# Kernel tuning notes

Hardware: AMD Instinct MI355X
Metric: run time of the kernel (lower is better)

Reference implementation:

```python
import jax, jax.numpy as jnp
import numpy as np

N = 65536      # num ref nodes
M = 65536      # num query nodes
E = 1572864    # num edges (avg degree 24)
K0 = 27        # num kernels (3x3x3 neighborhood)
D1 = 64        # input channels
D2 = 64        # output channels


def setup_inputs() -> dict:
    key = jax.random.key(0)
    k1, k2, k3, k4, k5, k6 = jax.random.split(key, 6)
    # kernel init mirrors initialize_kernel_weight (uniform in [-bound, bound])
    fan_in = D1 * K0
    gain = float(np.sqrt(2.0 / (1.0 + 5.0)))  # leaky_relu gain with slope sqrt(5)
    std = gain / np.sqrt(fan_in)
    bound = float(np.sqrt(3.0) * std)
    kernel = jax.random.uniform(k1, (K0, D1, D2), minval=-bound, maxval=bound, dtype=jnp.float32)
    ref_feat = jax.random.normal(k2, (N, D1), dtype=jnp.float32)
    e_kernel = jax.random.randint(k3, (E,), 0, K0)
    e_ref = jax.random.randint(k4, (E,), 0, N)
    e_query = jax.random.randint(k5, (E,), 0, M)
    e_weight = jax.random.uniform(k6, (E,), dtype=jnp.float32)
    return {
        "kernel": kernel,
        "ref_feat": ref_feat,
        "e_kernel": e_kernel,
        "e_ref": e_ref,
        "e_query": e_query,
        "num_queries": M,
        "e_weight": e_weight,
    }


def reference(kernel, ref_feat, e_kernel, e_ref, e_query, num_queries, e_weight):
    # Math of MessagePassing.forward:
    #   query_feat[m] = sum_{edges e: e_query[e]==m} w_e * (ref_feat[e_ref[e]] @ kernel[e_kernel[e]])
    # Efficient form: precompute each node's transform under every kernel
    # (N*K0*D1*D2 dense GEMM), then gather per edge and scatter-reduce.
    transformed = jnp.einsum('nd,kdo->nko', ref_feat, kernel)   # [N, K0, D2]
    msgs = transformed[e_ref, e_kernel] * e_weight[:, None]      # [E, D2]
    query_feat = jax.ops.segment_sum(msgs, e_query, num_segments=num_queries)  # [M, D2]
    return query_feat
```

## Files before the change

kernel.cpp:

```cpp
#include <hip/hip_runtime.h>

#define DIN 64
#define DOUT 64
#define MAXK 32

typedef __bf16 bf16x8 __attribute__((ext_vector_type(8)));
typedef float  f32x4  __attribute__((ext_vector_type(4)));

static __device__ inline unsigned short f2b(float x) {
    return __builtin_bit_cast(unsigned short, (__bf16)x);
}
static __device__ inline float b2f(unsigned short u) {
    return __uint_as_float(((unsigned int)u) << 16);
}


__global__ void conv_w_kernel(const float* __restrict__ W,
                              unsigned short* __restrict__ Wt, int total) {
    int i = blockIdx.x * blockDim.x + threadIdx.x;
    if (i < total) {
        int j    = i & 7;
        int lane = (i >> 3) & 63;
        int h    = (i >> 9) & 1;
        int t    = (i >> 10) & 3;
        int k    = i >> 12;
        int col  = lane & 15;
        int quad = lane >> 4;
        int d1 = h * 32 + quad * 8 + j;
        int d2 = t * 16 + col;
        Wt[i] = f2b(W[(k * 64 + d1) * 64 + d2]);
    }
}


__global__ __launch_bounds__(256) void phaseA_kernel(
    const float* __restrict__ ref,
    const unsigned short* __restrict__ Wt,
    unsigned short* __restrict__ T,
    int K0, int Nn)
{
    const int lane = threadIdx.x & 63;
    const int wid  = threadIdx.x >> 6;
    const int col  = lane & 15;
    const int quad = lane >> 4;
    const int n0   = blockIdx.x * 64 + wid * 16;
    const int row  = n0 + col;

    __shared__ __align__(16) char ldsbuf[4][16 * 144];
    char* buf = ldsbuf[wid];

    const float* rp = ref + (size_t)row * 64;
    f32x4 r0 = *reinterpret_cast<const f32x4*>(rp + quad * 8);
    f32x4 r1 = *reinterpret_cast<const f32x4*>(rp + quad * 8 + 4);
    f32x4 r2 = *reinterpret_cast<const f32x4*>(rp + 32 + quad * 8);
    f32x4 r3 = *reinterpret_cast<const f32x4*>(rp + 32 + quad * 8 + 4);
    bf16x8 b0, b1;
    #pragma unroll
    for (int i = 0; i < 4; ++i) {
        b0[i]     = (__bf16)r0[i];
        b0[4 + i] = (__bf16)r1[i];
        b1[i]     = (__bf16)r2[i];
        b1[4 + i] = (__bf16)r3[i];
    }

    const int rrow = lane >> 2;
    const int rq   = lane & 3;

    for (int k = 0; k < K0; ++k) {
        const unsigned short* Wk = Wt + (size_t)k * 4096;
        #pragma unroll
        for (int t = 0; t < 4; ++t) {
            const unsigned short* ap = Wk + (size_t)t * 1024 + lane * 8;
            bf16x8 a0 = *reinterpret_cast<const bf16x8*>(ap);
            bf16x8 a1 = *reinterpret_cast<const bf16x8*>(ap + 512);
            f32x4 c = {0.f, 0.f, 0.f, 0.f};
            c = __builtin_amdgcn_mfma_f32_16x16x32_bf16(a0, b0, c, 0, 0, 0);
            c = __builtin_amdgcn_mfma_f32_16x16x32_bf16(a1, b1, c, 0, 0, 0);
            unsigned int lo = (unsigned int)f2b(c[0]) | ((unsigned int)f2b(c[1]) << 16);
            unsigned int hi = (unsigned int)f2b(c[2]) | ((unsigned int)f2b(c[3]) << 16);
            *reinterpret_cast<uint2*>(buf + col * 144 + t * 32 + quad * 8) =
                make_uint2(lo, hi);
        }
        uint4 v0 = *reinterpret_cast<const uint4*>(buf + rrow * 144 + rq * 32);
        uint4 v1 = *reinterpret_cast<const uint4*>(buf + rrow * 144 + rq * 32 + 16);
        size_t gbase = ((size_t)k * Nn + n0 + rrow) * 64 + rq * 16;
        *reinterpret_cast<uint4*>(T + gbase)     = v0;
        *reinterpret_cast<uint4*>(T + gbase + 8) = v1;
    }
}


__global__ void p1_hist_kernel(const int* __restrict__ eq, int E,
                               int* __restrict__ qcount) {
    __shared__ int l[256];
    l[threadIdx.x] = 0;
    __syncthreads();
    int stride = gridDim.x * blockDim.x;
    for (int i = blockIdx.x * blockDim.x + threadIdx.x; i < E; i += stride)
        atomicAdd(&l[((unsigned)eq[i]) >> 8], 1);
    __syncthreads();
    int v = l[threadIdx.x];
    if (v) atomicAdd(&qcount[threadIdx.x], v);
}

__global__ void p1_scan_kernel(const int* __restrict__ qcount,
                               int* __restrict__ gbase, int* __restrict__ gcursor,
                               int* __restrict__ qstart, int NB, int M, int E) {
    __shared__ int sh[256];
    int t = threadIdx.x;
    int v = (t < NB) ? qcount[t] : 0;
    sh[t] = v;
    __syncthreads();
    #pragma unroll
    for (int o = 1; o < 256; o <<= 1) {
        int x = (t >= o) ? sh[t - o] : 0;
        __syncthreads();
        sh[t] += x;
        __syncthreads();
    }
    int ex = sh[t] - v;
    if (t < NB) { gbase[t] = ex; gcursor[t] = ex; }
    if (t == 0) qstart[M] = E;
}

__global__ __launch_bounds__(256) void p1_scatter_kernel(
    const int* __restrict__ eq, const int* __restrict__ er,
    const int* __restrict__ ek, const float* __restrict__ ew,
    int E, int* __restrict__ gcursor, uint2* __restrict__ tmp)
{
    __shared__ int bin[256];
    __shared__ int base[256];
    const int t = threadIdx.x;
    bin[t] = 0;
    __syncthreads();
    const int i0 = blockIdx.x * 4096;
    unsigned key[16];
    unsigned rank[16];
    uint2 pay[16];
    #pragma unroll
    for (int u = 0; u < 16; ++u) {
        int i = i0 + u * 256 + t;
        if (i < E) {
            int q = eq[i];
            unsigned b = ((unsigned)q) >> 8;
            key[u] = b;
            rank[u] = atomicAdd(&bin[b], 1);
            pay[u] = make_uint2((unsigned)er[i] | ((unsigned)ek[i] << 16) |
                                ((unsigned)(q & 255) << 21),
                                __float_as_uint(ew[i]));
        } else {
            key[u] = 0xFFFFFFFFu;
        }
    }
    __syncthreads();
    int c = bin[t];
    if (c) base[t] = atomicAdd(&gcursor[t], c);
    __syncthreads();
    #pragma unroll
    for (int u = 0; u < 16; ++u) {
        if (key[u] != 0xFFFFFFFFu)
            tmp[(size_t)base[key[u]] + rank[u]] = pay[u];
    }
}

__global__ __launch_bounds__(256) void p2_kernel(
    const uint2* __restrict__ tmp, const int* __restrict__ gbase,
    const int* __restrict__ qcount, uint2* __restrict__ rec,
    int* __restrict__ qstart)
{
    __shared__ int fine[256];
    __shared__ int foff[256];
    const int b = blockIdx.x;
    const int t = threadIdx.x;
    const int s = gbase[b];
    const int L = qcount[b];
    fine[t] = 0;
    __syncthreads();
    for (int i = t; i < L; i += 256)
        atomicAdd(&fine[(tmp[s + i].x >> 21) & 255], 1);
    __syncthreads();
    int v = fine[t];
    __syncthreads();
    #pragma unroll
    for (int o = 1; o < 256; o <<= 1) {
        int x = (t >= o) ? fine[t - o] : 0;
        __syncthreads();
        fine[t] += x;
        __syncthreads();
    }
    foff[t] = fine[t] - v;
    qstart[b * 256 + t] = s + foff[t];
    __syncthreads();
    fine[t] = 0;
    __syncthreads();
    for (int i = t; i < L; i += 256) {
        uint2 p = tmp[s + i];
        unsigned fb = (p.x >> 21) & 255;
        int r = atomicAdd(&fine[fb], 1);
        rec[(size_t)s + foff[fb] + r] = p;
    }
}


__global__ __launch_bounds__(256) void phaseB_kernel(
    const unsigned short* __restrict__ T,
    const uint2* __restrict__ rec,
    const int* __restrict__ qstart,
    float* __restrict__ out, int Nn)
{
    const int lane = threadIdx.x & 63;
    const int wid  = threadIdx.x >> 6;
    const int q    = blockIdx.x * 4 + wid;

    int beg = qstart[q];
    int end = qstart[q + 1];
    float acc = 0.f;

    int j = beg;
    for (; j + 3 < end; j += 4) {
        uint2 v0 = rec[j];
        uint2 v1 = rec[j + 1];
        uint2 v2 = rec[j + 2];
        uint2 v3 = rec[j + 3];
        unsigned m0 = __builtin_amdgcn_readfirstlane(v0.x);
        unsigned m1 = __builtin_amdgcn_readfirstlane(v1.x);
        unsigned m2 = __builtin_amdgcn_readfirstlane(v2.x);
        unsigned m3 = __builtin_amdgcn_readfirstlane(v3.x);
        float w0 = __uint_as_float(__builtin_amdgcn_readfirstlane(v0.y));
        float w1 = __uint_as_float(__builtin_amdgcn_readfirstlane(v1.y));
        float w2 = __uint_as_float(__builtin_amdgcn_readfirstlane(v2.y));
        float w3 = __uint_as_float(__builtin_amdgcn_readfirstlane(v3.y));
        unsigned short t0 = T[((size_t)((m0 >> 16) & 31) * Nn + (m0 & 0xFFFFu)) * 64 + lane];
        unsigned short t1 = T[((size_t)((m1 >> 16) & 31) * Nn + (m1 & 0xFFFFu)) * 64 + lane];
        unsigned short t2 = T[((size_t)((m2 >> 16) & 31) * Nn + (m2 & 0xFFFFu)) * 64 + lane];
        unsigned short t3 = T[((size_t)((m3 >> 16) & 31) * Nn + (m3 & 0xFFFFu)) * 64 + lane];
        acc = fmaf(w0, b2f(t0), acc);
        acc = fmaf(w1, b2f(t1), acc);
        acc = fmaf(w2, b2f(t2), acc);
        acc = fmaf(w3, b2f(t3), acc);
    }
    for (; j < end; ++j) {
        uint2 v0 = rec[j];
        unsigned m0 = __builtin_amdgcn_readfirstlane(v0.x);
        float w0 = __uint_as_float(__builtin_amdgcn_readfirstlane(v0.y));
        acc = fmaf(w0, b2f(T[((size_t)((m0 >> 16) & 31) * Nn + (m0 & 0xFFFFu)) * 64 + lane]), acc);
    }
    out[(size_t)q * 64 + lane] = acc;
}


__global__ void hist_kernel(const int* __restrict__ ek, int E, int* __restrict__ counts) {
    __shared__ int l[MAXK];
    if (threadIdx.x < MAXK) l[threadIdx.x] = 0;
    __syncthreads();
    int stride = gridDim.x * blockDim.x;
    for (int i = blockIdx.x * blockDim.x + threadIdx.x; i < E; i += stride)
        atomicAdd(&l[ek[i]], 1);
    __syncthreads();
    if (threadIdx.x < MAXK) {
        int v = l[threadIdx.x];
        if (v) atomicAdd(&counts[threadIdx.x], v);
    }
}

__global__ void scan_kernel(const int* __restrict__ counts, int K,
                            int* __restrict__ start, int* __restrict__ cursor) {
    if (threadIdx.x == 0 && blockIdx.x == 0) {
        int acc = 0;
        for (int k = 0; k < K; ++k) {
            start[k] = acc;
            cursor[k] = acc;
            acc += counts[k];
        }
    }
}

__global__ void scatter_kernel(const int* __restrict__ ek, int E,
                               int* __restrict__ cursor, int* __restrict__ sorted) {
    __shared__ int lcnt[MAXK], lbase[MAXK], lpos[MAXK];
    if (threadIdx.x < MAXK) { lcnt[threadIdx.x] = 0; lpos[threadIdx.x] = 0; }
    __syncthreads();
    int i = blockIdx.x * blockDim.x + threadIdx.x;
    int k = 0;
    bool valid = (i < E);
    if (valid) { k = ek[i]; atomicAdd(&lcnt[k], 1); }
    __syncthreads();
    if (threadIdx.x < MAXK) {
        int v = lcnt[threadIdx.x];
        if (v) lbase[threadIdx.x] = atomicAdd(&cursor[threadIdx.x], v);
    }
    __syncthreads();
    if (valid) {
        int slot = lbase[k] + atomicAdd(&lpos[k], 1);
        sorted[slot] = i;
    }
}

__global__ __launch_bounds__(256) void mp_bucket_kernel(
    const float* __restrict__ W, const float* __restrict__ ref,
    const int* __restrict__ e_ref, const int* __restrict__ e_query,
    const float* __restrict__ e_weight, const int* __restrict__ sorted,
    const int* __restrict__ start, const int* __restrict__ counts,
    float* __restrict__ out)
{
    const int k = blockIdx.y;
    const int lane = threadIdx.x & 63;
    const int wid = threadIdx.x >> 6;

    float wreg[DIN];
    const float* Wk = W + k * DIN * DOUT;
    #pragma unroll
    for (int d = 0; d < DIN; ++d) wreg[d] = Wk[d * DOUT + lane];

    const int s = start[k];
    const int c = counts[k];
    const int nwaves = gridDim.x * 4;

    for (int i = blockIdx.x * 4 + wid; i < c; i += nwaves) {
        int eid = __builtin_amdgcn_readfirstlane(sorted[s + i]);
        int r = e_ref[eid];
        int q = e_query[eid];
        float w = e_weight[eid];
        const float* row = ref + r * DIN;
        float a0 = 0.f, a1 = 0.f, a2 = 0.f, a3 = 0.f;
        #pragma unroll
        for (int d = 0; d < DIN; d += 4) {
            a0 += row[d + 0] * wreg[d + 0];
            a1 += row[d + 1] * wreg[d + 1];
            a2 += row[d + 2] * wreg[d + 2];
            a3 += row[d + 3] * wreg[d + 3];
        }
        atomicAdd(&out[q * DOUT + lane], ((a0 + a1) + (a2 + a3)) * w);
    }
}


extern "C" void kernel_launch(void* const* d_in, const int* in_sizes, int n_in,
                              void* d_out, int out_size, void* d_ws, size_t ws_size,
                              hipStream_t stream) {
    const float* W        = (const float*)d_in[0];
    const float* ref      = (const float*)d_in[1];
    const int*   e_kernel = (const int*)d_in[2];
    const int*   e_ref    = (const int*)d_in[3];
    const int*   e_query  = (const int*)d_in[4];
    const float* e_weight = (const float*)d_in[6];

    const int K0 = in_sizes[0] / (DIN * DOUT);
    const int N  = in_sizes[1] / DIN;
    const int E  = in_sizes[2];
    const int M  = out_size / DOUT;
    const int KD = K0 * 64;
    const int NB = M / 256;

    float* out = (float*)d_out;

    size_t off = 0;
    auto alloc = [&](size_t bytes, size_t align) {
        off = (off + align - 1) / align * align;
        size_t r = off; off += bytes; return r;
    };
    size_t o_tmp     = alloc((size_t)E * 8, 16);
    size_t o_rec     = alloc((size_t)E * 8, 16);
    size_t o_qstart  = alloc((size_t)(M + 1) * 4, 4);
    size_t o_qcount  = alloc(256 * 4, 4);
    size_t o_gbase   = alloc(256 * 4, 4);
    size_t o_gcursor = alloc(256 * 4, 4);
    size_t o_wt      = alloc((size_t)K0 * 4096 * 2, 16);
    size_t o_T       = alloc((size_t)N * KD * 2, 16);
    size_t needA = off;

    bool planA_ok = (ws_size >= needA) && (M % 256 == 0) && (NB >= 1) && (NB <= 256) &&
                    (N % 64 == 0) && (N <= 65536) && (K0 <= 32);

    if (planA_ok) {
        char* ws = (char*)d_ws;
        uint2* tmp           = (uint2*)(ws + o_tmp);
        uint2* rec           = (uint2*)(ws + o_rec);
        int*  qstart         = (int*)(ws + o_qstart);
        int*  qcount         = (int*)(ws + o_qcount);
        int*  gbase          = (int*)(ws + o_gbase);
        int*  gcursor        = (int*)(ws + o_gcursor);
        unsigned short* Wt   = (unsigned short*)(ws + o_wt);
        unsigned short* T    = (unsigned short*)(ws + o_T);

        conv_w_kernel<<<(K0 * 4096 + 255) / 256, 256, 0, stream>>>(W, Wt, K0 * 4096);

        hipMemsetAsync(qcount, 0, 256 * 4, stream);
        p1_hist_kernel<<<512, 256, 0, stream>>>(e_query, E, qcount);
        p1_scan_kernel<<<1, 256, 0, stream>>>(qcount, gbase, gcursor, qstart, NB, M, E);
        p1_scatter_kernel<<<(E + 4095) / 4096, 256, 0, stream>>>(e_query, e_ref, e_kernel,
                                                                 e_weight, E, gcursor, tmp);
        p2_kernel<<<NB, 256, 0, stream>>>(tmp, gbase, qcount, rec, qstart);

        phaseA_kernel<<<N / 64, 256, 0, stream>>>(ref, Wt, T, K0, N);

        phaseB_kernel<<<M / 4, 256, 0, stream>>>(T, rec, qstart, out, N);
    } else {
        hipMemsetAsync(out, 0, (size_t)out_size * sizeof(float), stream);
        size_t needB = (size_t)(96 + E) * sizeof(int);
        if (ws_size >= needB) {
            int* ws_i   = (int*)d_ws;
            int* counts = ws_i;
            int* start  = ws_i + 32;
            int* cursor = ws_i + 64;
            int* sorted = ws_i + 96;
            hipMemsetAsync(counts, 0, 96 * sizeof(int), stream);
            hist_kernel<<<512, 256, 0, stream>>>(e_kernel, E, counts);
            scan_kernel<<<1, 64, 0, stream>>>(counts, K0, start, cursor);
            scatter_kernel<<<(E + 255) / 256, 256, 0, stream>>>(e_kernel, E, cursor, sorted);
            dim3 grid(64, K0);
            mp_bucket_kernel<<<grid, 256, 0, stream>>>(W, ref, e_ref, e_query, e_weight,
                                                       sorted, start, counts, out);
        }
    }
}
```

Baseline: 293.0 us.

## Fuse per-node transform into edge-gather kernel, bucketing edges by query tile and kernel

Drops the precomputed N×K0×64 transformed table. Edges are now sorted by (query tile of 32, kernel index), and a fused kernel gathers bf16 ref rows and runs MFMA against that kernel's weights for each group of 16 edges. Weighted results are scatter-added into a 32×64 LDS accumulator with atomics. This removes the large table write and the per-edge gather of table rows, but it costs about one 64×64 GEMM per edge instead of per node, plus LDS atomic contention and partial MFMA tiles.

```diff
diff --git a/kernel.cpp b/kernel.cpp
--- a/kernel.cpp
+++ b/kernel.cpp
@@ -9,9 +9,6 @@
 
 static __device__ inline unsigned short f2b(float x) {
     return __builtin_bit_cast(unsigned short, (__bf16)x);
-}
-static __device__ inline float b2f(unsigned short u) {
-    return __uint_as_float(((unsigned int)u) << 16);
 }
 
 
@@ -32,60 +29,14 @@
     }
 }
 
-
-__global__ __launch_bounds__(256) void phaseA_kernel(
-    const float* __restrict__ ref,
-    const unsigned short* __restrict__ Wt,
-    unsigned short* __restrict__ T,
-    int K0, int Nn)
-{
-    const int lane = threadIdx.x & 63;
-    const int wid  = threadIdx.x >> 6;
-    const int col  = lane & 15;
-    const int quad = lane >> 4;
-    const int n0   = blockIdx.x * 64 + wid * 16;
-    const int row  = n0 + col;
-
-    __shared__ __align__(16) char ldsbuf[4][16 * 144];
-    char* buf = ldsbuf[wid];
-
-    const float* rp = ref + (size_t)row * 64;
-    f32x4 r0 = *reinterpret_cast<const f32x4*>(rp + quad * 8);
-    f32x4 r1 = *reinterpret_cast<const f32x4*>(rp + quad * 8 + 4);
-    f32x4 r2 = *reinterpret_cast<const f32x4*>(rp + 32 + quad * 8);
-    f32x4 r3 = *reinterpret_cast<const f32x4*>(rp + 32 + quad * 8 + 4);
-    bf16x8 b0, b1;
-    #pragma unroll
-    for (int i = 0; i < 4; ++i) {
-        b0[i]     = (__bf16)r0[i];
-        b0[4 + i] = (__bf16)r1[i];
-        b1[i]     = (__bf16)r2[i];
-        b1[4 + i] = (__bf16)r3[i];
-    }
-
-    const int rrow = lane >> 2;
-    const int rq   = lane & 3;
-
-    for (int k = 0; k < K0; ++k) {
-        const unsigned short* Wk = Wt + (size_t)k * 4096;
-        #pragma unroll
-        for (int t = 0; t < 4; ++t) {
-            const unsigned short* ap = Wk + (size_t)t * 1024 + lane * 8;
-            bf16x8 a0 = *reinterpret_cast<const bf16x8*>(ap);
-            bf16x8 a1 = *reinterpret_cast<const bf16x8*>(ap + 512);
-            f32x4 c = {0.f, 0.f, 0.f, 0.f};
-            c = __builtin_amdgcn_mfma_f32_16x16x32_bf16(a0, b0, c, 0, 0, 0);
-            c = __builtin_amdgcn_mfma_f32_16x16x32_bf16(a1, b1, c, 0, 0, 0);
-            unsigned int lo = (unsigned int)f2b(c[0]) | ((unsigned int)f2b(c[1]) << 16);
-            unsigned int hi = (unsigned int)f2b(c[2]) | ((unsigned int)f2b(c[3]) << 16);
-            *reinterpret_cast<uint2*>(buf + col * 144 + t * 32 + quad * 8) =
-                make_uint2(lo, hi);
-        }
-        uint4 v0 = *reinterpret_cast<const uint4*>(buf + rrow * 144 + rq * 32);
-        uint4 v1 = *reinterpret_cast<const uint4*>(buf + rrow * 144 + rq * 32 + 16);
-        size_t gbase = ((size_t)k * Nn + n0 + rrow) * 64 + rq * 16;
-        *reinterpret_cast<uint4*>(T + gbase)     = v0;
-        *reinterpret_cast<uint4*>(T + gbase + 8) = v1;
+__global__ void conv_ref_kernel(const float* __restrict__ src,
+                                ushort* __restrict__ dst, int n4) {
+    int i = blockIdx.x * blockDim.x + threadIdx.x;
+    if (i < n4) {
+        f32x4 v = *reinterpret_cast<const f32x4*>(src + i * 4);
+        ushort4 o;
+        o.x = f2b(v[0]); o.y = f2b(v[1]); o.z = f2b(v[2]); o.w = f2b(v[3]);
+        *reinterpret_cast<ushort4*>(dst + i * 4) = o;
     }
 }
 
@@ -105,7 +56,7 @@
 
 __global__ void p1_scan_kernel(const int* __restrict__ qcount,
                                int* __restrict__ gbase, int* __restrict__ gcursor,
-                               int* __restrict__ qstart, int NB, int M, int E) {
+                               int NB) {
     __shared__ int sh[256];
     int t = threadIdx.x;
     int v = (t < NB) ? qcount[t] : 0;
@@ -120,7 +71,6 @@
     }
     int ex = sh[t] - v;
     if (t < NB) { gbase[t] = ex; gcursor[t] = ex; }
-    if (t == 0) qstart[M] = E;
 }
 
 __global__ __launch_bounds__(256) void p1_scatter_kernel(
@@ -166,7 +116,7 @@
 __global__ __launch_bounds__(256) void p2_kernel(
     const uint2* __restrict__ tmp, const int* __restrict__ gbase,
     const int* __restrict__ qcount, uint2* __restrict__ rec,
-    int* __restrict__ qstart)
+    int* __restrict__ tkstart, int* __restrict__ tkcount)
 {
     __shared__ int fine[256];
     __shared__ int foff[256];
@@ -176,8 +126,10 @@
     const int L = qcount[b];
     fine[t] = 0;
     __syncthreads();
-    for (int i = t; i < L; i += 256)
-        atomicAdd(&fine[(tmp[s + i].x >> 21) & 255], 1);
+    for (int i = t; i < L; i += 256) {
+        unsigned x = tmp[s + i].x;
+        atomicAdd(&fine[((x >> 26) & 7) * 32 + ((x >> 16) & 31)], 1);
+    }
     __syncthreads();
     int v = fine[t];
     __syncthreads();
@@ -189,63 +141,89 @@
         __syncthreads();
     }
     foff[t] = fine[t] - v;
-    qstart[b * 256 + t] = s + foff[t];
+    tkstart[b * 256 + t] = s + foff[t];
+    tkcount[b * 256 + t] = v;
     __syncthreads();
     fine[t] = 0;
     __syncthreads();
     for (int i = t; i < L; i += 256) {
         uint2 p = tmp[s + i];
-        unsigned fb = (p.x >> 21) & 255;
+        unsigned fb = ((p.x >> 26) & 7) * 32 + ((p.x >> 16) & 31);
         int r = atomicAdd(&fine[fb], 1);
         rec[(size_t)s + foff[fb] + r] = p;
     }
 }
 
 
-__global__ __launch_bounds__(256) void phaseB_kernel(
-    const unsigned short* __restrict__ T,
+__global__ __launch_bounds__(256) void fused_kernel(
+    const ushort* __restrict__ refb,
+    const unsigned short* __restrict__ Wt,
     const uint2* __restrict__ rec,
-    const int* __restrict__ qstart,
-    float* __restrict__ out, int Nn)
+    const int* __restrict__ tkstart, const int* __restrict__ tkcount,
+    float* __restrict__ out, int K0)
 {
-    const int lane = threadIdx.x & 63;
-    const int wid  = threadIdx.x >> 6;
-    const int q    = blockIdx.x * 4 + wid;
-
-    int beg = qstart[q];
-    int end = qstart[q + 1];
-    float acc = 0.f;
-
-    int j = beg;
-    for (; j + 3 < end; j += 4) {
-        uint2 v0 = rec[j];
-        uint2 v1 = rec[j + 1];
-        uint2 v2 = rec[j + 2];
-        uint2 v3 = rec[j + 3];
-        unsigned m0 = __builtin_amdgcn_readfirstlane(v0.x);
-        unsigned m1 = __builtin_amdgcn_readfirstlane(v1.x);
-        unsigned m2 = __builtin_amdgcn_readfirstlane(v2.x);
-        unsigned m3 = __builtin_amdgcn_readfirstlane(v3.x);
-        float w0 = __uint_as_float(__builtin_amdgcn_readfirstlane(v0.y));
-        float w1 = __uint_as_float(__builtin_amdgcn_readfirstlane(v1.y));
-        float w2 = __uint_as_float(__builtin_amdgcn_readfirstlane(v2.y));
-        float w3 = __uint_as_float(__builtin_amdgcn_readfirstlane(v3.y));
-        unsigned short t0 = T[((size_t)((m0 >> 16) & 31) * Nn + (m0 & 0xFFFFu)) * 64 + lane];
-        unsigned short t1 = T[((size_t)((m1 >> 16) & 31) * Nn + (m1 & 0xFFFFu)) * 64 + lane];
-        unsigned short t2 = T[((size_t)((m2 >> 16) & 31) * Nn + (m2 & 0xFFFFu)) * 64 + lane];
-        unsigned short t3 = T[((size_t)((m3 >> 16) & 31) * Nn + (m3 & 0xFFFFu)) * 64 + lane];
-        acc = fmaf(w0, b2f(t0), acc);
-        acc = fmaf(w1, b2f(t1), acc);
-        acc = fmaf(w2, b2f(t2), acc);
-        acc = fmaf(w3, b2f(t3), acc);
-    }
-    for (; j < end; ++j) {
-        uint2 v0 = rec[j];
-        unsigned m0 = __builtin_amdgcn_readfirstlane(v0.x);
-        float w0 = __uint_as_float(__builtin_amdgcn_readfirstlane(v0.y));
-        acc = fmaf(w0, b2f(T[((size_t)((m0 >> 16) & 31) * Nn + (m0 & 0xFFFFu)) * 64 + lane]), acc);
-    }
-    out[(size_t)q * 64 + lane] = acc;
+    __shared__ float acc[32 * 65];
+    const int tid  = threadIdx.x;
+    const int lane = tid & 63;
+    const int wid  = tid >> 6;
+    const int col  = lane & 15;
+    const int quad = lane >> 4;
+    const int tile = blockIdx.x;
+    const int binbase = tile * 32;
+
+    for (int i = tid; i < 32 * 65; i += 256) acc[i] = 0.f;
+    __syncthreads();
+
+    for (int k = wid; k < K0; k += 4) {
+        int s   = tkstart[binbase + k];
+        int cnt = tkcount[binbase + k];
+        if (cnt == 0) continue;
+
+        const unsigned short* wp = Wt + (size_t)k * 4096;
+        bf16x8 bw[4][2];
+        #pragma unroll
+        for (int t = 0; t < 4; ++t) {
+            const unsigned short* ap = wp + t * 1024 + lane * 8;
+            bw[t][0] = *reinterpret_cast<const bf16x8*>(ap);
+            bw[t][1] = *reinterpret_cast<const bf16x8*>(ap + 512);
+        }
+
+        for (int i0 = 0; i0 < cnt; i0 += 16) {
+            uint2 rv = make_uint2(0u, 0u);
+            if (lane < 16 && i0 + lane < cnt) rv = rec[(size_t)s + i0 + lane];
+
+            unsigned rx = (unsigned)__shfl((int)rv.x, col);
+            int r = rx & 0xFFFF;
+            const ushort* rp = refb + (size_t)r * 64 + quad * 8;
+            bf16x8 a0 = *reinterpret_cast<const bf16x8*>(rp);
+            bf16x8 a1 = *reinterpret_cast<const bf16x8*>(rp + 32);
+
+            float wv[4]; int qv[4];
+            #pragma unroll
+            for (int g = 0; g < 4; ++g) {
+                int m = quad * 4 + g;
+                unsigned mx = (unsigned)__shfl((int)rv.x, m);
+                unsigned mw = (unsigned)__shfl((int)rv.y, m);
+                qv[g] = (mx >> 21) & 31;
+                wv[g] = __uint_as_float(mw);
+            }
+
+            #pragma unroll
+            for (int t = 0; t < 4; ++t) {
+                f32x4 c = {0.f, 0.f, 0.f, 0.f};
+                c = __builtin_amdgcn_mfma_f32_16x16x32_bf16(a0, bw[t][0], c, 0, 0, 0);
+                c = __builtin_amdgcn_mfma_f32_16x16x32_bf16(a1, bw[t][1], c, 0, 0, 0);
+                #pragma unroll
+                for (int g = 0; g < 4; ++g)
+                    atomicAdd(&acc[qv[g] * 65 + t * 16 + col], wv[g] * c[g]);
+            }
+        }
+    }
+    __syncthreads();
+
+    size_t gb = (size_t)tile * 32 * 64;
+    for (int i = tid; i < 32 * 64; i += 256)
+        out[gb + i] = acc[(i >> 6) * 65 + (i & 63)];
 }
 
 
@@ -349,7 +327,6 @@
     const int N  = in_sizes[1] / DIN;
     const int E  = in_sizes[2];
     const int M  = out_size / DOUT;
-    const int KD = K0 * 64;
     const int NB = M / 256;
 
     float* out = (float*)d_out;
@@ -361,12 +338,13 @@
     };
     size_t o_tmp     = alloc((size_t)E * 8, 16);
     size_t o_rec     = alloc((size_t)E * 8, 16);
-    size_t o_qstart  = alloc((size_t)(M + 1) * 4, 4);
     size_t o_qcount  = alloc(256 * 4, 4);
     size_t o_gbase   = alloc(256 * 4, 4);
     size_t o_gcursor = alloc(256 * 4, 4);
+    size_t o_tks     = alloc((size_t)NB * 256 * 4, 4);
+    size_t o_tkc     = alloc((size_t)NB * 256 * 4, 4);
     size_t o_wt      = alloc((size_t)K0 * 4096 * 2, 16);
-    size_t o_T       = alloc((size_t)N * KD * 2, 16);
+    size_t o_refb    = alloc((size_t)N * 64 * 2, 16);
     size_t needA = off;
 
     bool planA_ok = (ws_size >= needA) && (M % 256 == 0) && (NB >= 1) && (NB <= 256) &&
@@ -376,25 +354,25 @@
         char* ws = (char*)d_ws;
         uint2* tmp           = (uint2*)(ws + o_tmp);
         uint2* rec           = (uint2*)(ws + o_rec);
-        int*  qstart         = (int*)(ws + o_qstart);
         int*  qcount         = (int*)(ws + o_qcount);
         int*  gbase          = (int*)(ws + o_gbase);
         int*  gcursor        = (int*)(ws + o_gcursor);
+        int*  tkstart        = (int*)(ws + o_tks);
+        int*  tkcount        = (int*)(ws + o_tkc);
         unsigned short* Wt   = (unsigned short*)(ws + o_wt);
-        unsigned short* T    = (unsigned short*)(ws + o_T);
+        ushort* refb         = (ushort*)(ws + o_refb);
 
         conv_w_kernel<<<(K0 * 4096 + 255) / 256, 256, 0, stream>>>(W, Wt, K0 * 4096);
+        conv_ref_kernel<<<(N * 16 + 255) / 256, 256, 0, stream>>>(ref, refb, N * 16);
 
         hipMemsetAsync(qcount, 0, 256 * 4, stream);
         p1_hist_kernel<<<512, 256, 0, stream>>>(e_query, E, qcount);
-        p1_scan_kernel<<<1, 256, 0, stream>>>(qcount, gbase, gcursor, qstart, NB, M, E);
+        p1_scan_kernel<<<1, 256, 0, stream>>>(qcount, gbase, gcursor, NB);
         p1_scatter_kernel<<<(E + 4095) / 4096, 256, 0, stream>>>(e_query, e_ref, e_kernel,
                                                                  e_weight, E, gcursor, tmp);
-        p2_kernel<<<NB, 256, 0, stream>>>(tmp, gbase, qcount, rec, qstart);
-
-        phaseA_kernel<<<N / 64, 256, 0, stream>>>(ref, Wt, T, K0, N);
-
-        phaseB_kernel<<<M / 4, 256, 0, stream>>>(T, rec, qstart, out, N);
+        p2_kernel<<<NB, 256, 0, stream>>>(tmp, gbase, qcount, rec, tkstart, tkcount);
+
+        fused_kernel<<<M / 32, 256, 0, stream>>>(refb, Wt, rec, tkstart, tkcount, out, K0);
     } else {
         hipMemsetAsync(out, 0, (size_t)out_size * sizeof(float), stream);
         size_t needB = (size_t)(96 + E) * sizeof(int);
```

Measured after the change: 805.3 us. +174.9%, slower.
